# Performance work log

Measured on AMD Instinct MI355X. Metric: run time of the kernel, lower is better.

Reference implementation:

```python
import jax, jax.numpy as jnp
import numpy as np

B, T, C = 2, 2048, 2048
H, KVH, D = 16, 4, 128
EPS = 1.1920929e-07  # torch.finfo(float32).eps, default for F.rms_norm


def setup_inputs() -> dict:
    key = jax.random.key(0)
    ks = jax.random.split(key, 5)
    x = jax.random.normal(ks[0], (B, T, C), jnp.float32)
    # standard RoPE angle tables, shaped to broadcast over [B, T, heads, D/2]
    half = D // 2
    inv_freq = 1.0 / (10000.0 ** (np.arange(half, dtype=np.float64) / half))
    ang = np.arange(T, dtype=np.float64)[:, None] * inv_freq[None, :]
    cos = jnp.asarray(np.cos(ang), jnp.float32)[None, :, None, :]
    sin = jnp.asarray(np.sin(ang), jnp.float32)[None, :, None, :]
    s = C ** -0.5
    Wq = jax.random.normal(ks[1], (H * D, C), jnp.float32) * s
    Wk = jax.random.normal(ks[2], (KVH * D, C), jnp.float32) * s
    Wv = jax.random.normal(ks[3], (KVH * D, C), jnp.float32) * s
    Wo = jax.random.normal(ks[4], (C, C), jnp.float32) * s
    return {"x": x, "cos": cos, "sin": sin, "Wq": Wq, "Wk": Wk, "Wv": Wv, "Wo": Wo}


def _rope(x, cos, sin):
    d = x.shape[-1] // 2
    x1, x2 = x[..., :d], x[..., d:]
    return jnp.concatenate([x1 * cos + x2 * sin, -x1 * sin + x2 * cos], axis=-1)


def _rmsnorm(x):
    return x * jax.lax.rsqrt(jnp.mean(x * x, axis=-1, keepdims=True) + EPS)


def reference(x, cos, sin, Wq, Wk, Wv, Wo):
    Bx, Tx, Cx = x.shape
    q = (x @ Wq.T).reshape(Bx, Tx, H, D)
    k = (x @ Wk.T).reshape(Bx, Tx, KVH, D)
    v = (x @ Wv.T).reshape(Bx, Tx, KVH, D)
    q = _rmsnorm(_rope(q, cos, sin))
    k = _rmsnorm(_rope(k, cos, sin))
    # [B, heads, T, D]
    q = q.transpose(0, 2, 1, 3)
    k = k.transpose(0, 2, 1, 3)
    v = v.transpose(0, 2, 1, 3)
    groups = H // KVH  # GQA: replicate kv heads
    k = jnp.repeat(k, groups, axis=1)
    v = jnp.repeat(v, groups, axis=1)
    scale = 1.0 / jnp.sqrt(jnp.asarray(D, x.dtype))
    scores = jnp.einsum('bhqd,bhkd->bhqk', q, k) * scale
    causal = jnp.tril(jnp.ones((Tx, Tx), dtype=bool))
    scores = jnp.where(causal, scores, jnp.finfo(scores.dtype).min)
    att = jax.nn.softmax(scores, axis=-1)
    y = jnp.einsum('bhqk,bhkd->bhqd', att, v)
    y = y.transpose(0, 2, 1, 3).reshape(Bx, Tx, H * D)
    return y @ Wo.T
```

## Files before the change

### kernel.cpp

```cpp
#include <hip/hip_runtime.h>
#include <hip/hip_bf16.h>

typedef unsigned short u16t;
typedef unsigned int   u32t;
typedef float  f32x4 __attribute__((ext_vector_type(4)));
typedef short  s16x8 __attribute__((ext_vector_type(8)));
typedef unsigned int u32x4 __attribute__((ext_vector_type(4)));
typedef float  f4 __attribute__((ext_vector_type(4)));

#define BB 2
#define TT 2048
#define CC 2048
#define HH 16
#define KVHN 4
#define DD 128
#define EPSV 1.1920929e-07f
#define SCALE 0.08838834764831845f
#define MFIX 12.0f

__device__ __forceinline__ float b2f(u16t u){ union{u32t i; float f;} x; x.i=((u32t)u)<<16; return x.f; }
__device__ __forceinline__ u16t f2b(float f){ union{float f; u32t i;} x; x.f=f; u32t r = x.i + 0x7fffu + ((x.i>>16)&1u); return (u16t)(r>>16); }
__device__ __forceinline__ u32t pk2(float a, float b){
    __hip_bfloat162 h = __float22bfloat162_rn(make_float2(a,b));
    u32t r; __builtin_memcpy(&r,&h,4); return r;
}
__device__ __forceinline__ s16x8 ldf(const u16t* p){ s16x8 r; __builtin_memcpy(&r,p,16); return r; }
__device__ __forceinline__ void st16(u16t* p, u32x4 v){ __builtin_memcpy(p,&v,16); }
__device__ __forceinline__ u32x4 ldg16(const u16t* p){ u32x4 r; __builtin_memcpy(&r,p,16); return r; }

typedef const __attribute__((address_space(1))) unsigned int ga_u32;
typedef __attribute__((address_space(3))) unsigned int ls_u32;
__device__ __forceinline__ void gl16(const u16t* g, u16t* l) {
    __builtin_amdgcn_global_load_lds((ga_u32*)(unsigned long long)(g),
                                     (ls_u32*)(unsigned int)(unsigned long long)(l),
                                     16, 0, 0);
}

#define BARRIER() __builtin_amdgcn_s_barrier()
#define SCHEDB()  __builtin_amdgcn_sched_barrier(0)
#define WAITLG0() asm volatile("s_waitcnt lgkmcnt(0)" ::: "memory")
#define WAITLG4() asm volatile("s_waitcnt lgkmcnt(4)" ::: "memory")
#define WAITVM8() asm volatile("s_waitcnt vmcnt(8)" ::: "memory")
#define WAITVM6() asm volatile("s_waitcnt vmcnt(6)" ::: "memory")
#define WAITVM5() asm volatile("s_waitcnt vmcnt(5)" ::: "memory")
#define WAITVM0() asm volatile("s_waitcnt vmcnt(0)" ::: "memory")

__global__ __launch_bounds__(256) void cvt_kernel(
    const float* __restrict__ x,  const float* __restrict__ wq,
    const float* __restrict__ wk, const float* __restrict__ wv,
    const float* __restrict__ wo,
    u16t* __restrict__ xb, u16t* __restrict__ wqb, u16t* __restrict__ wkb,
    u16t* __restrict__ wvb, u16t* __restrict__ wob)
{
    size_t g = (size_t)blockIdx.x * 256 + threadIdx.x;
    const float* src; u16t* dst; size_t off;
    if      (g < 1048576) { src = x;  dst = xb;  off = g; }
    else if (g < 1572864) { src = wq; dst = wqb; off = g - 1048576; }
    else if (g < 1703936) { src = wk; dst = wkb; off = g - 1572864; }
    else if (g < 1835008) { src = wv; dst = wvb; off = g - 1703936; }
    else                  { src = wo; dst = wob; off = g - 1835008; }
    f4 a = *(const f4*)(src + off*8);
    f4 b = *(const f4*)(src + off*8 + 4);
    u32x4 o = { pk2(a[0],a[1]), pk2(a[2],a[3]), pk2(b[0],b[1]), pk2(b[2],b[3]) };
    st16(dst + off*8, o);
}

template<int NF, bool BSW>
__device__ __forceinline__ void gemm256(
    const u16t* __restrict__ aPanel, const u16t* __restrict__ bPanel,
    u16t* lds, f32x4 (&acc)[4][NF], const int tid)
{
    constexpr int BQ = NF/2;
    constexpr int BS = NF/4;
    u16t* Abuf[2] = { lds,         lds + 16384 };
    u16t* Bbuf[2] = { lds + 32768, lds + 32768 + NF*2048 };
    const int w = tid>>6, quad = (tid>>4)&3, l15 = tid&15;
    const int wr = (w>>1)*64, wc = (w&1)*(BQ*16);
    const int gcol = (((tid&7) ^ ((tid>>3)&7)) << 3);
    const u16t* aB  = aPanel + (size_t)(tid>>3)*CC + gcol;
    const u16t* bBr = bPanel + (size_t)(tid>>3)*CC + gcol;

    #pragma unroll
    for (int i=0;i<4;++i)
        #pragma unroll
        for (int j=0;j<NF;++j)
            #pragma unroll
            for (int r=0;r<4;++r) acc[i][j][r] = 0.f;

    #pragma unroll
    for (int i=0;i<4;++i) gl16(aB + (size_t)(i*64)*CC, Abuf[0] + (i*512+tid)*8);
    #pragma unroll
    for (int s=0;s<2*BS;++s){
        const int ss = BSW ? ((s==1)?2:((s==2)?1:s)) : s;
        gl16(bBr + (size_t)(ss*64)*CC, Bbuf[0] + (s*512+tid)*8);
    }
    SCHEDB();
    #pragma unroll
    for (int i=0;i<4;++i) gl16(aB + (size_t)(i*64)*CC + 64, Abuf[1] + (i*512+tid)*8);
    #pragma unroll
    for (int s=0;s<BS;++s){
        const int ss = BSW ? ((s==1)?2:s) : s;
        gl16(bBr + (size_t)(ss*64)*CC + 64, Bbuf[1] + (s*512+tid)*8);
    }

    s16x8 af0[4], af1[4], bf[BQ];

    #pragma unroll 2
    for (int kt=0; kt<32; ++kt){
        const u16t* Ac = Abuf[kt&1];
        const u16t* Bc = Bbuf[kt&1];
        u16t* An = Abuf[kt&1];
        u16t* Bn = Bbuf[kt&1];
        u16t* Bo = Bbuf[(kt+1)&1];
        if (kt == 31) { WAITVM0(); }
        else { if constexpr (NF==8) { WAITVM6(); } else { WAITVM5(); } }
        SCHEDB();
        BARRIER();

        #pragma unroll
        for (int mi=0;mi<4;++mi){
            const int row = wr + mi*16 + l15;
            af0[mi] = ldf(Ac + row*64 + ((quad ^ (row&7))<<3));
        }
        #pragma unroll
        for (int ni=0;ni<BQ;++ni){
            const int row = wc + ni*16 + l15;
            bf[ni] = ldf(Bc + row*64 + ((quad ^ (row&7))<<3));
        }
        #pragma unroll
        for (int mi=0;mi<4;++mi){
            const int row = wr + mi*16 + l15;
            af1[mi] = ldf(Ac + row*64 + (((4|quad) ^ (row&7))<<3));
        }
        SCHEDB();
        BARRIER();
        WAITLG4();
        SCHEDB();
        __builtin_amdgcn_s_setprio(1);
        #pragma unroll
        for (int mi=0;mi<4;++mi)
            #pragma unroll
            for (int ni=0;ni<BQ;++ni)
                acc[mi][ni] = __builtin_amdgcn_mfma_f32_16x16x32_bf16(
                    af0[mi], bf[ni], acc[mi][ni], 0,0,0);
        __builtin_amdgcn_s_setprio(0);

        #pragma unroll
        for (int ni=0;ni<BQ;++ni){
            const int row = wc + ni*16 + l15;
            bf[ni] = ldf(Bc + row*64 + (((4|quad) ^ (row&7))<<3));
        }
        if (kt < 31){
            #pragma unroll
            for (int s=0;s<BS;++s){
                const int sl = BS + s;
                const int ss = BSW ? ((sl==2)?1:sl) : sl;
                gl16(bBr + (size_t)(ss*64)*CC + (kt+1)*64, Bo + (sl*512+tid)*8);
            }
        }
        SCHEDB();
        BARRIER();
        WAITLG0();
        SCHEDB();
        __builtin_amdgcn_s_setprio(1);
        #pragma unroll
        for (int mi=0;mi<4;++mi)
            #pragma unroll
            for (int ni=0;ni<BQ;++ni)
                acc[mi][ni] = __builtin_amdgcn_mfma_f32_16x16x32_bf16(
                    af1[mi], bf[ni], acc[mi][ni], 0,0,0);
        __builtin_amdgcn_s_setprio(0);

        #pragma unroll
        for (int ni=0;ni<BQ;++ni){
            const int row = NF*16 + wc + ni*16 + l15;
            bf[ni] = ldf(Bc + row*64 + ((quad ^ (row&7))<<3));
        }
        if (kt < 30){
            #pragma unroll
            for (int i=0;i<4;++i)
                gl16(aB + (size_t)(i*64)*CC + (kt+2)*64, An + (i*512+tid)*8);
        }
        SCHEDB();
        BARRIER();
        WAITLG0();
        SCHEDB();
        __builtin_amdgcn_s_setprio(1);
        #pragma unroll
        for (int mi=0;mi<4;++mi)
            #pragma unroll
            for (int ni=0;ni<BQ;++ni)
                acc[mi][BQ+ni] = __builtin_amdgcn_mfma_f32_16x16x32_bf16(
                    af0[mi], bf[ni], acc[mi][BQ+ni], 0,0,0);
        __builtin_amdgcn_s_setprio(0);

        #pragma unroll
        for (int ni=0;ni<BQ;++ni){
            const int row = NF*16 + wc + ni*16 + l15;
            bf[ni] = ldf(Bc + row*64 + (((4|quad) ^ (row&7))<<3));
        }
        if (kt < 30){
            #pragma unroll
            for (int s=0;s<BS;++s){
                const int ss = BSW ? ((s==1)?2:s) : s;
                gl16(bBr + (size_t)(ss*64)*CC + (kt+2)*64, Bn + (s*512+tid)*8);
            }
        }
        SCHEDB();
        BARRIER();
        WAITLG0();
        SCHEDB();
        __builtin_amdgcn_s_setprio(1);
        #pragma unroll
        for (int mi=0;mi<4;++mi)
            #pragma unroll
            for (int ni=0;ni<BQ;++ni)
                acc[mi][BQ+ni] = __builtin_amdgcn_mfma_f32_16x16x32_bf16(
                    af1[mi], bf[ni], acc[mi][BQ+ni], 0,0,0);
        __builtin_amdgcn_s_setprio(0);
    }
}

__global__ __launch_bounds__(512,2) void qkv_kernel(
    const u16t* __restrict__ xb, const u16t* __restrict__ wqb,
    const u16t* __restrict__ wkb, const u16t* __restrict__ wvb,
    const float* __restrict__ cosp, const float* __restrict__ sinp,
    u16t* __restrict__ qws, u16t* __restrict__ kws, u16t* __restrict__ vtw)
{
    __shared__ __align__(16) u16t lds[65536];
    const int tid = threadIdx.x;
    const int bx = blockIdx.x, by = blockIdx.y;
    const int m0 = bx*256;

    int type, headbase; const u16t* W;
    if (by < 8)       { type=0; W = wqb + (size_t)by*256*CC;      headbase = by*2; }
    else if (by < 10) { type=1; W = wkb + (size_t)(by-8)*256*CC;  headbase = (by-8)*2; }
    else              { type=2; W = wvb + (size_t)(by-10)*256*CC; headbase = (by-10)*2; }

    f32x4 acc[4][8];
    gemm256<8,true>(xb + (size_t)m0*CC, W, lds, acc, tid);

    const int w = tid>>6, quad = (tid>>4)&3, l15 = tid&15;
    const int wr = (w>>1)*64, wn = w&1;
    const int head = headbase + wn;
    const int bb = bx>>3;
    const int ttb = (m0 + wr) & 2047;

    if (type == 2){
        u16t* vb = vtw + (size_t)(bb*KVHN+head)*DD*TT;
        #pragma unroll
        for (int mi=0;mi<4;++mi){
            const int tt = ttb + mi*16 + quad*4;
            #pragma unroll
            for (int ni=0;ni<8;++ni){
                const int d = ((ni>>2)*64) + ((ni&3)*16) + l15;
                u16t o[4];
                #pragma unroll
                for (int r=0;r<4;++r) o[r] = f2b(acc[mi][ni][r]);
                __builtin_memcpy(vb + (size_t)d*TT + tt, o, 8);
            }
        }
    } else {
        u16t* dst = (type==0) ? (qws + (size_t)(bb*HH+head)*TT*DD)
                              : (kws + (size_t)(bb*KVHN+head)*TT*DD);
        #pragma unroll
        for (int mi=0;mi<4;++mi){
            const int tt0 = ttb + mi*16 + quad*4;
            float ss[4] = {0.f,0.f,0.f,0.f};
            #pragma unroll
            for (int ni=0;ni<8;++ni)
                #pragma unroll
                for (int r=0;r<4;++r) ss[r] += acc[mi][ni][r]*acc[mi][ni][r];
            float rms[4];
            #pragma unroll
            for (int r=0;r<4;++r){
                float s = ss[r];
                s += __shfl_xor(s, 1, 16);
                s += __shfl_xor(s, 2, 16);
                s += __shfl_xor(s, 4, 16);
                s += __shfl_xor(s, 8, 16);
                rms[r] = rsqrtf(s*(1.f/128.f) + EPSV);
            }
            #pragma unroll
            for (int ni=0;ni<4;++ni){
                const int j = ni*16 + l15;
                #pragma unroll
                for (int r=0;r<4;++r){
                    const int tt = tt0 + r;
                    const float c = cosp[tt*64 + j];
                    const float s = sinp[tt*64 + j];
                    const float z1 = acc[mi][ni][r], z2 = acc[mi][ni+4][r];
                    dst[(size_t)tt*DD + j]      = f2b((z1*c + z2*s)*rms[r]);
                    dst[(size_t)tt*DD + j + 64] = f2b((z2*c - z1*s)*rms[r]);
                }
            }
        }
    }
}

__global__ __launch_bounds__(256,2) void attn_kernel(
    const u16t* __restrict__ qws, const u16t* __restrict__ kws,
    const u16t* __restrict__ vtw, u16t* __restrict__ yws)
{
    __shared__ __align__(16) u16t lds[40960];
    u16t* Ps = lds + 32768;

    const int tid = threadIdx.x;
    const int w = tid>>6, lane = tid&63, quad = lane>>4, l15 = lane&15;
    const int bx = blockIdx.x, h = blockIdx.y, b = blockIdx.z, kvh = h>>2;

    const int qti    = b ? bx : (15 - bx);
    const int qwbase = qti*128 + w*32;
    const int nkt    = (qti+1)*2;

    const u16t* kb = kws + (size_t)(b*KVHN+kvh)*TT*DD;
    const u16t* vb = vtw + (size_t)(b*KVHN+kvh)*DD*TT;

    const int krow = tid>>4;
    const int kcg  = (tid&15) ^ ((tid>>4)&7);
    const int vrow = tid>>3;
    const int vcg  = (tid&7)  ^ ((tid>>3)&7);

    const u16t* qp = qws + ((size_t)(b*HH+h)*TT + qwbase + l15)*DD + quad*8;
    s16x8 qf[2][4];
    #pragma unroll
    for (int mi=0;mi<2;++mi)
        #pragma unroll
        for (int kq=0;kq<4;++kq)
            qf[mi][kq] = ldf(qp + (size_t)mi*16*DD + kq*32);
    SCHEDB();

    {
        u16t* Kd = lds;        u16t* Vd = lds + 16384;
        #pragma unroll
        for (int j=0;j<4;++j)
            gl16(kb + (size_t)(krow + j*16)*DD + kcg*8,      Kd + (j*256+tid)*8);
        #pragma unroll
        for (int j=0;j<4;++j)
            gl16(vb + (size_t)(vrow + j*32)*TT + vcg*8,      Vd + (j*256+tid)*8);
        SCHEDB();
        Kd = lds + 8192;       Vd = lds + 24576;
        #pragma unroll
        for (int j=0;j<4;++j)
            gl16(kb + (size_t)(64 + krow + j*16)*DD + kcg*8, Kd + (j*256+tid)*8);
        #pragma unroll
        for (int j=0;j<4;++j)
            gl16(vb + (size_t)(vrow + j*32)*TT + 64 + vcg*8, Vd + (j*256+tid)*8);
    }

    f32x4 o_[2][8];
    float l_[2][4];
    #pragma unroll
    for (int mi=0;mi<2;++mi){
        #pragma unroll
        for (int r=0;r<4;++r) l_[mi][r] = 0.f;
        #pragma unroll
        for (int n8=0;n8<8;++n8)
            #pragma unroll
            for (int r=0;r<4;++r) o_[mi][n8][r] = 0.f;
    }

    const int swz = (l15&7)<<3;

    for (int kt=0; kt<nkt; ++kt){
        const int k0 = kt*64;
        if (kt+1 == nkt) { WAITVM0(); } else { WAITVM8(); }
        SCHEDB();
        BARRIER();
        if (k0 <= qwbase + 31) {
            const u16t* Ks = (kt&1) ? (lds + 8192)  : lds;
            const u16t* Vt = (kt&1) ? (lds + 24576) : (lds + 16384);

            f32x4 s[2][4];
            #pragma unroll
            for (int mi=0;mi<2;++mi)
                #pragma unroll
                for (int ni=0;ni<4;++ni)
                    #pragma unroll
                    for (int r=0;r<4;++r) s[mi][ni][r] = 0.f;
            #pragma unroll
            for (int kq=0;kq<4;++kq){
                s16x8 kf[4];
                #pragma unroll
                for (int ni=0;ni<4;++ni)
                    kf[ni] = ldf(Ks + (ni*16+l15)*128 + (((kq*4+quad)<<3) ^ swz));
                __builtin_amdgcn_s_setprio(1);
                #pragma unroll
                for (int mi=0;mi<2;++mi)
                    #pragma unroll
                    for (int ni=0;ni<4;++ni)
                        s[mi][ni] = __builtin_amdgcn_mfma_f32_16x16x32_bf16(qf[mi][kq], kf[ni], s[mi][ni], 0,0,0);
                __builtin_amdgcn_s_setprio(0);
            }

            const bool need_mask = (k0 + 63) > qwbase;
            #pragma unroll
            for (int mi=0;mi<2;++mi){
                const int qrow = qwbase + mi*16 + quad*4;
                #pragma unroll
                for (int ni=0;ni<4;++ni){
                    const int kcol = k0 + ni*16 + l15;
                    #pragma unroll
                    for (int r=0;r<4;++r){
                        float p = __expf(__builtin_fmaf(s[mi][ni][r], SCALE, -MFIX));
                        if (need_mask && kcol > qrow + r) p = 0.f;
                        l_[mi][r] += p;
                        const int rw = w*32 + mi*16 + quad*4 + r;
                        Ps[rw*64 + ((ni*16+l15) ^ (((quad*4+r)&7)<<3))] = f2b(p);
                    }
                }
            }

            #pragma unroll
            for (int ks=0;ks<2;++ks){
                s16x8 pf[2];
                #pragma unroll
                for (int mi=0;mi<2;++mi)
                    pf[mi] = ldf(Ps + (w*32+mi*16+l15)*64 + (((ks*4+quad)<<3) ^ swz));
                __builtin_amdgcn_s_setprio(1);
                #pragma unroll
                for (int n8=0;n8<8;++n8){
                    s16x8 vf = ldf(Vt + (n8*16+l15)*64 + (((ks*4+quad)<<3) ^ swz));
                    #pragma unroll
                    for (int mi=0;mi<2;++mi)
                        o_[mi][n8] = __builtin_amdgcn_mfma_f32_16x16x32_bf16(pf[mi], vf, o_[mi][n8], 0,0,0);
                }
                __builtin_amdgcn_s_setprio(0);
            }
        }
        BARRIER();
        if (kt+2 < nkt){
            const int kn = (kt+2)*64;
            u16t* Kd = (kt&1) ? (lds + 8192)  : lds;
            u16t* Vd = (kt&1) ? (lds + 24576) : (lds + 16384);
            #pragma unroll
            for (int j=0;j<4;++j)
                gl16(kb + (size_t)(kn + krow + j*16)*DD + kcg*8, Kd + (j*256+tid)*8);
            #pragma unroll
            for (int j=0;j<4;++j)
                gl16(vb + (size_t)(vrow + j*32)*TT + kn + vcg*8, Vd + (j*256+tid)*8);
        }
    }

    #pragma unroll
    for (int mi=0;mi<2;++mi){
        const int qrow = qwbase + mi*16 + quad*4;
        float inv[4];
        #pragma unroll
        for (int r=0;r<4;++r){
            float lt = l_[mi][r];
            lt += __shfl_xor(lt,1,16);
            lt += __shfl_xor(lt,2,16);
            lt += __shfl_xor(lt,4,16);
            lt += __shfl_xor(lt,8,16);
            inv[r] = 1.f/lt;
        }
        #pragma unroll
        for (int n8=0;n8<8;++n8)
            #pragma unroll
            for (int r=0;r<4;++r)
                yws[((size_t)(b*TT + qrow + r))*2048 + h*DD + n8*16 + l15] = f2b(o_[mi][n8][r]*inv[r]);
    }
}

__global__ __launch_bounds__(512,2) void oproj_kernel(
    const u16t* __restrict__ y, const u16t* __restrict__ wob, float* __restrict__ out)
{
    __shared__ __align__(16) u16t lds[49152];
    const int tid = threadIdx.x;
    const int m0 = blockIdx.x*256, n0 = blockIdx.y*128;

    f32x4 acc[4][4];
    gemm256<4,false>(y + (size_t)m0*CC, wob + (size_t)n0*CC, lds, acc, tid);

    const int w = tid>>6, quad = (tid>>4)&3, l15 = tid&15;
    const int wr = (w>>1)*64, wcq = (w&1)*32;
    #pragma unroll
    for (int mi=0;mi<4;++mi){
        const int m = m0 + wr + mi*16 + quad*4;
        #pragma unroll
        for (int ni=0;ni<4;++ni){
            const int n = n0 + ((ni>>1)*64) + wcq + ((ni&1)*16) + l15;
            #pragma unroll
            for (int r=0;r<4;++r)
                out[(size_t)(m+r)*CC + n] = acc[mi][ni][r];
        }
    }
}

extern "C" void kernel_launch(void* const* d_in, const int* in_sizes, int n_in,
                              void* d_out, int out_size, void* d_ws, size_t ws_size,
                              hipStream_t stream) {
    const float* x    = (const float*)d_in[0];
    const float* cosp = (const float*)d_in[1];
    const float* sinp = (const float*)d_in[2];
    const float* Wq   = (const float*)d_in[3];
    const float* Wk   = (const float*)d_in[4];
    const float* Wv   = (const float*)d_in[5];
    const float* Wo   = (const float*)d_in[6];

    u16t* ws  = (u16t*)d_ws;
    u16t* xb  = ws;
    u16t* wqb = xb  + 8388608;
    u16t* wkb = wqb + 4194304;
    u16t* wvb = wkb + 1048576;
    u16t* wob = wvb + 1048576;
    u16t* qws = wob + 4194304;
    u16t* kws = qws + 8388608;
    u16t* vtw = kws + 2097152;
    u16t* yws = xb;
    float* out = (float*)d_out;

    cvt_kernel<<<dim3(9216), 256, 0, stream>>>(x, Wq, Wk, Wv, Wo, xb, wqb, wkb, wvb, wob);
    qkv_kernel<<<dim3(16, 12), 512, 0, stream>>>(xb, wqb, wkb, wvb, cosp, sinp, qws, kws, vtw);
    attn_kernel<<<dim3(16, 16, 2), 256, 0, stream>>>(qws, kws, vtw, yws);
    oproj_kernel<<<dim3(16, 16), 512, 0, stream>>>(yws, wob, out);
}
```

Baseline: 300.6 us.

## Software-pipeline QK^T of next KV tile with softmax and PV of current tile

Restructures the attention inner loop so the QK^T MFMAs for tile kt+1 are issued before the softmax and PV work of tile kt, with scores carried across iterations in registers. K and V prefetches are split and timed separately: K is issued right after the top barrier and V after the bottom barrier, with vmcnt waits adjusted to match. The aim is to overlap exp/mask/LDS-store latency with matrix work and to ease the wait on global loads. In exchange it costs an extra score tile of registers, and it drops the per-warp skip of fully masked tiles, so some warps now compute tiles that are entirely masked out.

```diff
diff --git a/kernel.cpp b/kernel.cpp
--- a/kernel.cpp
+++ b/kernel.cpp
@@ -40,9 +40,11 @@
 #define SCHEDB()  __builtin_amdgcn_sched_barrier(0)
 #define WAITLG0() asm volatile("s_waitcnt lgkmcnt(0)" ::: "memory")
 #define WAITLG4() asm volatile("s_waitcnt lgkmcnt(4)" ::: "memory")
+#define WAITVM12() asm volatile("s_waitcnt vmcnt(12)" ::: "memory")
 #define WAITVM8() asm volatile("s_waitcnt vmcnt(8)" ::: "memory")
 #define WAITVM6() asm volatile("s_waitcnt vmcnt(6)" ::: "memory")
 #define WAITVM5() asm volatile("s_waitcnt vmcnt(5)" ::: "memory")
+#define WAITVM4() asm volatile("s_waitcnt vmcnt(4)" ::: "memory")
 #define WAITVM0() asm volatile("s_waitcnt vmcnt(0)" ::: "memory")
 
 __global__ __launch_bounds__(256) void cvt_kernel(
@@ -329,20 +331,23 @@
         for (int kq=0;kq<4;++kq)
             qf[mi][kq] = ldf(qp + (size_t)mi*16*DD + kq*32);
     SCHEDB();
-
     {
-        u16t* Kd = lds;        u16t* Vd = lds + 16384;
+        u16t* Kd = lds;
         #pragma unroll
         for (int j=0;j<4;++j)
             gl16(kb + (size_t)(krow + j*16)*DD + kcg*8,      Kd + (j*256+tid)*8);
+        SCHEDB();
+        u16t* Vd = lds + 16384;
         #pragma unroll
         for (int j=0;j<4;++j)
             gl16(vb + (size_t)(vrow + j*32)*TT + vcg*8,      Vd + (j*256+tid)*8);
         SCHEDB();
-        Kd = lds + 8192;       Vd = lds + 24576;
+        Kd = lds + 8192;
         #pragma unroll
         for (int j=0;j<4;++j)
             gl16(kb + (size_t)(64 + krow + j*16)*DD + kcg*8, Kd + (j*256+tid)*8);
+        SCHEDB();
+        Vd = lds + 24576;
         #pragma unroll
         for (int j=0;j<4;++j)
             gl16(vb + (size_t)(vrow + j*32)*TT + 64 + vcg*8, Vd + (j*256+tid)*8);
@@ -362,55 +367,73 @@
 
     const int swz = (l15&7)<<3;
 
+    auto qk = [&](const u16t* Ks, f32x4 (&s)[2][4]) {
+        #pragma unroll
+        for (int mi=0;mi<2;++mi)
+            #pragma unroll
+            for (int ni=0;ni<4;++ni)
+                #pragma unroll
+                for (int r=0;r<4;++r) s[mi][ni][r] = 0.f;
+        #pragma unroll
+        for (int kq=0;kq<4;++kq){
+            s16x8 kf[4];
+            #pragma unroll
+            for (int ni=0;ni<4;++ni)
+                kf[ni] = ldf(Ks + (ni*16+l15)*128 + (((kq*4+quad)<<3) ^ swz));
+            __builtin_amdgcn_s_setprio(1);
+            #pragma unroll
+            for (int mi=0;mi<2;++mi)
+                #pragma unroll
+                for (int ni=0;ni<4;++ni)
+                    s[mi][ni] = __builtin_amdgcn_mfma_f32_16x16x32_bf16(qf[mi][kq], kf[ni], s[mi][ni], 0,0,0);
+            __builtin_amdgcn_s_setprio(0);
+        }
+    };
+
+    WAITVM12();
+    SCHEDB();
+    BARRIER();
+    f32x4 sc[2][4];
+    qk(lds, sc);
+
     for (int kt=0; kt<nkt; ++kt){
         const int k0 = kt*64;
-        if (kt+1 == nkt) { WAITVM0(); } else { WAITVM8(); }
-        SCHEDB();
-        BARRIER();
-        if (k0 <= qwbase + 31) {
-            const u16t* Ks = (kt&1) ? (lds + 8192)  : lds;
+        if (kt == nkt-1) { WAITVM0(); } else { WAITVM4(); }
+        SCHEDB();
+        BARRIER();
+
+        if (kt+2 < nkt){
+            u16t* Kd = (kt&1) ? (lds + 8192) : lds;
+            const int kn = (kt+2)*64;
+            #pragma unroll
+            for (int j=0;j<4;++j)
+                gl16(kb + (size_t)(kn + krow + j*16)*DD + kcg*8, Kd + (j*256+tid)*8);
+        }
+
+        f32x4 sn[2][4];
+        if (kt+1 < nkt)
+            qk(((kt+1)&1) ? (lds + 8192) : lds, sn);
+
+        const bool need_mask = (k0 + 63) > qwbase;
+        #pragma unroll
+        for (int mi=0;mi<2;++mi){
+            const int qrow = qwbase + mi*16 + quad*4;
+            #pragma unroll
+            for (int ni=0;ni<4;++ni){
+                const int kcol = k0 + ni*16 + l15;
+                #pragma unroll
+                for (int r=0;r<4;++r){
+                    float p = __expf(__builtin_fmaf(sc[mi][ni][r], SCALE, -MFIX));
+                    if (need_mask && kcol > qrow + r) p = 0.f;
+                    l_[mi][r] += p;
+                    const int rw = w*32 + mi*16 + quad*4 + r;
+                    Ps[rw*64 + ((ni*16+l15) ^ (((quad*4+r)&7)<<3))] = f2b(p);
+                }
+            }
+        }
+
+        {
             const u16t* Vt = (kt&1) ? (lds + 24576) : (lds + 16384);
-
-            f32x4 s[2][4];
-            #pragma unroll
-            for (int mi=0;mi<2;++mi)
-                #pragma unroll
-                for (int ni=0;ni<4;++ni)
-                    #pragma unroll
-                    for (int r=0;r<4;++r) s[mi][ni][r] = 0.f;
-            #pragma unroll
-            for (int kq=0;kq<4;++kq){
-                s16x8 kf[4];
-                #pragma unroll
-                for (int ni=0;ni<4;++ni)
-                    kf[ni] = ldf(Ks + (ni*16+l15)*128 + (((kq*4+quad)<<3) ^ swz));
-                __builtin_amdgcn_s_setprio(1);
-                #pragma unroll
-                for (int mi=0;mi<2;++mi)
-                    #pragma unroll
-                    for (int ni=0;ni<4;++ni)
-                        s[mi][ni] = __builtin_amdgcn_mfma_f32_16x16x32_bf16(qf[mi][kq], kf[ni], s[mi][ni], 0,0,0);
-                __builtin_amdgcn_s_setprio(0);
-            }
-
-            const bool need_mask = (k0 + 63) > qwbase;
-            #pragma unroll
-            for (int mi=0;mi<2;++mi){
-                const int qrow = qwbase + mi*16 + quad*4;
-                #pragma unroll
-                for (int ni=0;ni<4;++ni){
-                    const int kcol = k0 + ni*16 + l15;
-                    #pragma unroll
-                    for (int r=0;r<4;++r){
-                        float p = __expf(__builtin_fmaf(s[mi][ni][r], SCALE, -MFIX));
-                        if (need_mask && kcol > qrow + r) p = 0.f;
-                        l_[mi][r] += p;
-                        const int rw = w*32 + mi*16 + quad*4 + r;
-                        Ps[rw*64 + ((ni*16+l15) ^ (((quad*4+r)&7)<<3))] = f2b(p);
-                    }
-                }
-            }
-
             #pragma unroll
             for (int ks=0;ks<2;++ks){
                 s16x8 pf[2];
@@ -428,17 +451,22 @@
                 __builtin_amdgcn_s_setprio(0);
             }
         }
+
         BARRIER();
         if (kt+2 < nkt){
+            u16t* Vd = (kt&1) ? (lds + 24576) : (lds + 16384);
             const int kn = (kt+2)*64;
-            u16t* Kd = (kt&1) ? (lds + 8192)  : lds;
-            u16t* Vd = (kt&1) ? (lds + 24576) : (lds + 16384);
-            #pragma unroll
-            for (int j=0;j<4;++j)
-                gl16(kb + (size_t)(kn + krow + j*16)*DD + kcg*8, Kd + (j*256+tid)*8);
             #pragma unroll
             for (int j=0;j<4;++j)
                 gl16(vb + (size_t)(vrow + j*32)*TT + kn + vcg*8, Vd + (j*256+tid)*8);
+        }
+
+        if (kt+1 < nkt){
+            #pragma unroll
+            for (int mi=0;mi<2;++mi)
+                #pragma unroll
+                for (int ni=0;ni<4;++ni)
+                    sc[mi][ni] = sn[mi][ni];
         }
     }
 
```

After: 312.8 us. 4.1% more time.
